# Kernel optimization log

Hardware: AMD Instinct MI355X
Metric: run time of the kernel (lower is better)

## Reference

```python
import jax, jax.numpy as jnp
import numpy as np

B, S, V, NC3, ND = 128, 200, 64, 4000, 100


def setup_inputs() -> dict:
    key = jax.random.key(0)
    ks = jax.random.split(key, 20)
    s = 0.05
    n = lambda k, shp: jax.random.normal(k, shp, dtype=jnp.float32) * s
    return {
        "c3_seq": jax.random.randint(ks[0], (B, S), 0, NC3),
        "d_seq": jax.random.randint(ks[1], (B, S), 0, ND),
        "r_seq": jax.random.randint(ks[2], (B, S), 0, 2),
        "v_c3": n(ks[3], (V,)),
        "D_w": n(ks[4], (ND, 1)),
        "v_d": n(ks[5], (V,)),
        "R_w": n(ks[6], (2, V)),
        "W_ih": n(ks[7], (3 * V, 2 * V)),
        "W_hh": n(ks[8], (3 * V, V)),
        "b_ih": n(ks[9], (3 * V,)),
        "b_hh": n(ks[10], (3 * V,)),
        "l1_w1": n(ks[11], (V, V)),
        "l1_b1": n(ks[12], (V,)),
        "l1_w2": n(ks[13], (1, V)),
        "l1_b2": n(ks[14], (1,)),
        "l2_w1": n(ks[15], (V, 3 * V)),
        "l2_b1": n(ks[16], (V,)),
        "l2_w2": n(ks[17], (1, V)),
        "l2_b2": n(ks[18], (1,)),
    }


def _forward(c3_seq, d_seq, r_seq, v_c3, D_w, v_d, R_w, W_ih, W_hh, b_ih, b_hh,
             l1_w1, l1_b1, l1_w2, l1_b2, l2_w1, l2_b1, l2_w2, l2_b2):
    B_, S_ = c3_seq.shape
    V_ = v_c3.shape[0]
    gamma_seq = D_w[d_seq]                       # [B,S,1]
    v_d_seq = gamma_seq * v_d                    # [B,S,V]
    v_r_seq = R_w[r_seq]                         # [B,S,V]
    x = jnp.concatenate([v_d_seq, v_r_seq], axis=-1)  # [B,S,2V]
    xg = x @ W_ih.T + b_ih                       # precompute GRU input gates [B,S,3V]

    # time-major for scan
    tm = lambda a: jnp.swapaxes(a, 0, 1)
    xg_t, gamma_t = tm(xg), tm(gamma_seq[..., 0])
    r_t, c3_t = tm(r_seq), tm(c3_seq)
    vd_t, vr_t = tm(v_d_seq), tm(v_r_seq)
    rows = jnp.arange(B_)

    def mlp1(h):  # linear_1 (dropout = identity in eval)
        return (jax.nn.relu(h @ l1_w1.T + l1_b1) @ l1_w2.T + l1_b2)[:, 0]

    def mlp2(z):  # linear_2
        return (jax.nn.relu(z @ l2_w1.T + l2_b1) @ l2_w2.T + l2_b2)[:, 0]

    h0 = jnp.zeros((B_, V_), xg.dtype)
    alpha0 = jnp.zeros((B_,), xg.dtype)
    C3_init = jnp.zeros((B_, NC3), xg.dtype)

    def step(carry, inputs):
        h, alpha, C3 = carry
        xg_i, gamma, r, c3, vdi, vri = inputs
        # GRU cell (torch gate order: r, z, n)
        hg = h @ W_hh.T + b_hh
        rg = jax.nn.sigmoid(xg_i[:, :V_] + hg[:, :V_])
        zg = jax.nn.sigmoid(xg_i[:, V_:2 * V_] + hg[:, V_:2 * V_])
        ng = jnp.tanh(xg_i[:, 2 * V_:] + rg * hg[:, 2 * V_:])
        h = (1.0 - zg) * ng + zg * h
        # alpha update
        alpha_new = mlp1(h)
        cond = (alpha - gamma) >= 0
        alpha = jnp.where(r == 1,
                          jnp.where(cond, alpha_new, alpha),
                          jnp.where(cond, alpha, alpha_new))
        # gather -> tiny MLP -> scatter
        beta = C3[rows, c3]                              # [B]
        z = jnp.concatenate([beta[:, None] * v_c3, vdi, vri], axis=-1)  # [B,3V]
        new_c3 = mlp2(z)
        C3 = C3.at[rows, c3].set(new_c3)
        return (h, alpha, C3), (h, alpha, C3)

    _, (h_seq, alpha_seq, C3_seq) = jax.lax.scan(
        step, (h0, alpha0, C3_init), (xg_t, gamma_t, r_t, c3_t, vd_t, vr_t))
    return tm(alpha_seq), tm(h_seq), tm(C3_seq)


def reference(c3_seq, d_seq, r_seq, v_c3, D_w, v_d, R_w, W_ih, W_hh, b_ih, b_hh,
              l1_w1, l1_b1, l1_w2, l1_b2, l2_w1, l2_b1, l2_w2, l2_b2):
    return _forward(c3_seq, d_seq, r_seq, v_c3, D_w, v_d, R_w, W_ih, W_hh, b_ih, b_hh,
                    l1_w1, l1_b1, l1_w2, l1_b2, l2_w1, l2_b1, l2_w2, l2_b2)
```

## Files before the change

### kernel.cpp

```cpp
#include <hip/hip_runtime.h>
#include <math.h>

#define Bn 128
#define Sn 200
#define NC3n 4000
#define GRUB Bn
#define FILLB (Bn * 4)

__device__ __forceinline__ float fexp(float x) { return __builtin_amdgcn_exp2f(x * 1.44269504f); }
__device__ __forceinline__ float frcp(float x) { return __builtin_amdgcn_rcpf(x); }
__device__ __forceinline__ float fsig(float x) { return frcp(1.f + fexp(-x)); }
__device__ __forceinline__ float rlanef(float v, int k) {
    return __int_as_float(__builtin_amdgcn_readlane(__float_as_int(v), k));
}

#define UPD(q, cbase) { int d = cc - (cbase); if ((unsigned)d < 4u) { \
    q.x = (d==0)?v:q.x; q.y = (d==1)?v:q.y; q.z = (d==2)?v:q.z; q.w = (d==3)?v:q.w; } }

struct GruLds {
    float ring[2][16][64];
    float pPart[Sn][4];
    float hbc[4][64];
    float u[192], w0[192], w1[192];
    float hg[2][192];
    float gam[Sn];
    int   r[Sn];
};
struct FillLds {
    float gam[Sn], val[Sn];
    int   r[Sn], c3[Sn], succ[Sn], root[Sn];
    float A[64], Bv[64], C0[64], C1[64], W2[64];
    float l2b2;
};

__global__ __launch_bounds__(256, 2) void fused4_kernel(
    const int* __restrict__ c3_seq, const int* __restrict__ d_seq,
    const int* __restrict__ r_seq, const float* __restrict__ v_c3,
    const float* __restrict__ D_w, const float* __restrict__ v_d,
    const float* __restrict__ R_w, const float* __restrict__ W_ih,
    const float* __restrict__ W_hh, const float* __restrict__ b_ih,
    const float* __restrict__ b_hh,
    const float* __restrict__ l1_w1, const float* __restrict__ l1_b1,
    const float* __restrict__ l1_w2, const float* __restrict__ l1_b2,
    const float* __restrict__ l2_w1, const float* __restrict__ l2_b1,
    const float* __restrict__ l2_w2, const float* __restrict__ l2_b2,
    float* __restrict__ out_alpha, float* __restrict__ out_h,
    float* __restrict__ out_c3)
{
    __shared__ __align__(16) union { GruLds g; FillLds f; } S;

    const int tid = threadIdx.x;
    const int bid = blockIdx.x;

    if (bid < GRUB) {
        __builtin_amdgcn_s_setprio(1);
        const int b    = bid;
        const int role = tid >> 6;
        const int j    = tid & 63;

        if (tid < Sn) {
            S.g.gam[tid] = D_w[d_seq[b * Sn + tid]];
            S.g.r[tid]   = r_seq[b * Sn + tid];
        }
        if (tid < 192) {
            const float4* rp  = (const float4*)(W_ih + (size_t)tid * 128);
            const float4* vd4 = (const float4*)v_d;
            const float4* q04 = (const float4*)R_w;
            const float4* q14 = (const float4*)(R_w + 64);
            float u = 0.f, w0 = 0.f, w1 = 0.f;
            #pragma unroll 4
            for (int k = 0; k < 16; ++k) {
                float4 a  = rp[k];
                float4 bb = rp[16 + k];
                float4 vd = vd4[k], q0 = q04[k], q1 = q14[k];
                u  += a.x*vd.x + a.y*vd.y + a.z*vd.z + a.w*vd.w;
                w0 += bb.x*q0.x + bb.y*q0.y + bb.z*q0.z + bb.w*q0.w;
                w1 += bb.x*q1.x + bb.y*q1.y + bb.z*q1.z + bb.w*q1.w;
            }
            float bih = b_ih[tid];
            S.g.u[tid]  = u;
            S.g.w0[tid] = w0 + bih;
            S.g.w1[tid] = w1 + bih;
        }
        float w[64];
        {
            const float* src = (role < 3) ? (W_hh + (size_t)(role * 64 + j) * 64)
                                          : (l1_w1 + (size_t)j * 64);
            const float4* s4 = (const float4*)src;
            #pragma unroll
            for (int k = 0; k < 16; ++k) {
                float4 v = s4[k];
                w[4*k+0]=v.x; w[4*k+1]=v.y; w[4*k+2]=v.z; w[4*k+3]=v.w;
            }
        }
        float bown = 0.f, l1b = 0.f, l1w2v = 0.f;
        if (role < 3) {
            bown = b_hh[role * 64 + j];
            S.g.hg[0][role * 64 + j] = bown;
        } else {
            l1b = l1_b1[j]; l1w2v = l1_w2[j];
        }
        const float l1b2c = l1_b2[0];
        __syncthreads();

        const float uj  = S.g.u[j],  u1  = S.g.u[64+j],  u2  = S.g.u[128+j];
        const float w00 = S.g.w0[j], w01 = S.g.w0[64+j], w02 = S.g.w0[128+j];
        const float w10 = S.g.w1[j], w11 = S.g.w1[64+j], w12 = S.g.w1[128+j];

        float vh = 0.f;
        float* outh_base = out_h + (size_t)b * Sn * 64;
        const int rloc = 4 * role + (j >> 4);
        const int cloc = (j & 15) * 4;

        for (int t = 0; t < Sn; ++t) {
            if (t && (t & 15) == 0) {
                const int hb = ((t >> 4) & 1) ^ 1;
                float4 v4 = *(const float4*)&S.g.ring[hb][rloc][cloc];
                *(float4*)(outh_base + (size_t)(t - 16 + rloc) * 64 + cloc) = v4;
            }
            const int buf = t & 1;
            float gam = S.g.gam[t];
            int   r   = S.g.r[t];
            float hr = S.g.hg[buf][j], hz = S.g.hg[buf][64+j], hn = S.g.hg[buf][128+j];
            float rg = fsig(fmaf(gam, uj, r ? w10 : w00) + hr);
            float zg = fsig(fmaf(gam, u1, r ? w11 : w01) + hz);
            float e2 = fexp(2.f * (fmaf(gam, u2, r ? w12 : w02) + rg * hn));
            float ng = 1.f - 2.f * frcp(e2 + 1.f);
            vh = (1.f - zg) * ng + zg * vh;
            S.g.hbc[role][j] = vh;
            float4 hreg[16];
            #pragma unroll
            for (int k = 0; k < 16; ++k)
                hreg[k] = *(const float4*)&S.g.hbc[role][k * 4];
            __builtin_amdgcn_sched_barrier(0);
            float a0=0.f, a1=0.f, a2=0.f, a3=0.f;
            #pragma unroll
            for (int k = 0; k < 16; ++k) {
                a0 = fmaf(w[4*k+0], hreg[k].x, a0);
                a1 = fmaf(w[4*k+1], hreg[k].y, a1);
                a2 = fmaf(w[4*k+2], hreg[k].z, a2);
                a3 = fmaf(w[4*k+3], hreg[k].w, a3);
            }
            float dot = (a0 + a1) + (a2 + a3);
            if (role < 3) {
                S.g.hg[buf ^ 1][role * 64 + j] = bown + dot;
            } else {
                float p = fmaxf(dot + l1b, 0.f) * l1w2v;
                p += __shfl_xor(p, 1);
                p += __shfl_xor(p, 2);
                p += __shfl_xor(p, 4);
                p += __shfl_xor(p, 8);
                if ((j & 15) == 0) S.g.pPart[t][j >> 4] = p;
                S.g.ring[(t >> 4) & 1][t & 15][j] = vh;
            }
            __syncthreads();
        }
        if (role < 2) {
            float4 v4 = *(const float4*)&S.g.ring[0][rloc][cloc];
            *(float4*)(outh_base + (size_t)(192 + rloc) * 64 + cloc) = v4;
        }
        if (role == 3) {
            float4 pp0 = *(const float4*)&S.g.pPart[j][0];
            float4 pp1 = *(const float4*)&S.g.pPart[64 + j][0];
            float4 pp2 = *(const float4*)&S.g.pPart[128 + j][0];
            const int j3 = (j < 8) ? (192 + j) : 199;
            float4 pp3 = *(const float4*)&S.g.pPart[j3][0];
            float an0 = ((pp0.x+pp0.y)+(pp0.z+pp0.w)) + l1b2c;
            float an1 = ((pp1.x+pp1.y)+(pp1.z+pp1.w)) + l1b2c;
            float an2 = ((pp2.x+pp2.y)+(pp2.z+pp2.w)) + l1b2c;
            float an3 = ((pp3.x+pp3.y)+(pp3.z+pp3.w)) + l1b2c;
            float g0 = S.g.gam[j],       g1 = S.g.gam[64 + j];
            float g2 = S.g.gam[128 + j], g3 = S.g.gam[j3];
            int   r0 = S.g.r[j],         r1 = S.g.r[64 + j];
            int   r2 = S.g.r[128 + j],   r3 = S.g.r[j3];
            float alpha = 0.f;
            float* oa = out_alpha + b * Sn;
            for (int t = 0; t < Sn; ++t) {
                const int q = t >> 6, l = t & 63;
                float an, g; int rr;
                if (q == 0)      { an = rlanef(an0,l); g = rlanef(g0,l); rr = __builtin_amdgcn_readlane(r0,l); }
                else if (q == 1) { an = rlanef(an1,l); g = rlanef(g1,l); rr = __builtin_amdgcn_readlane(r1,l); }
                else if (q == 2) { an = rlanef(an2,l); g = rlanef(g2,l); rr = __builtin_amdgcn_readlane(r2,l); }
                else             { an = rlanef(an3,l); g = rlanef(g3,l); rr = __builtin_amdgcn_readlane(r3,l); }
                bool cond = (alpha - g) >= 0.f;
                alpha = rr ? (cond ? an : alpha) : (cond ? alpha : an);
                if (j == 0) oa[t] = alpha;
            }
        }
    } else {
        const int fb = bid - GRUB;
        const int b  = fb >> 2;
        const int qt = fb & 3;
        if (tid < Sn) {
            S.f.gam[tid] = D_w[d_seq[b*Sn + tid]];
            S.f.r[tid]   = r_seq[b*Sn + tid];
            S.f.c3[tid]  = c3_seq[b*Sn + tid];
        }
        if (tid < 64) {
            const float4* row4 = (const float4*)(l2_w1 + (size_t)tid * 192);
            const float4* vc4  = (const float4*)v_c3;
            const float4* vd4  = (const float4*)v_d;
            const float4* q04  = (const float4*)R_w;
            const float4* q14  = (const float4*)(R_w + 64);
            float a2=0.f, b2=0.f, c0=0.f, c1=0.f;
            #pragma unroll 4
            for (int k = 0; k < 16; ++k) {
                float4 ra = row4[k], rb = row4[16+k], rc = row4[32+k];
                float4 vc = vc4[k], vd = vd4[k], q0 = q04[k], q1 = q14[k];
                a2 += ra.x*vc.x + ra.y*vc.y + ra.z*vc.z + ra.w*vc.w;
                b2 += rb.x*vd.x + rb.y*vd.y + rb.z*vd.z + rb.w*vd.w;
                c0 += rc.x*q0.x + rc.y*q0.y + rc.z*q0.z + rc.w*q0.w;
                c1 += rc.x*q1.x + rc.y*q1.y + rc.z*q1.z + rc.w*q1.w;
            }
            S.f.A[tid]  = a2;
            S.f.Bv[tid] = b2;
            S.f.C0[tid] = c0 + l2_b1[tid];
            S.f.C1[tid] = c1 + l2_b1[tid];
            S.f.W2[tid] = l2_w2[tid];
        }
        if (tid == 0) S.f.l2b2 = l2_b2[0];
        __syncthreads();
        if (tid < Sn) {
            int c = S.f.c3[tid];
            int s = -1;
            for (int u = tid + 1; u < Sn; ++u)
                if (S.f.c3[u] == c) { s = u; break; }
            S.f.succ[tid] = s;
            int rt = 1;
            for (int u = 0; u < tid; ++u)
                if (S.f.c3[u] == c) { rt = 0; break; }
            S.f.root[tid] = rt;
        }
        __syncthreads();
        {
            const int g  = tid >> 4;
            const int l  = tid & 15;
            const int j0 = l * 4;
            float A0=S.f.A[j0],  A1=S.f.A[j0+1],  A2=S.f.A[j0+2],  A3=S.f.A[j0+3];
            float B0=S.f.Bv[j0], B1=S.f.Bv[j0+1], B2=S.f.Bv[j0+2], B3=S.f.Bv[j0+3];
            float C00=S.f.C0[j0],C01=S.f.C0[j0+1],C02=S.f.C0[j0+2],C03=S.f.C0[j0+3];
            float C10=S.f.C1[j0],C11=S.f.C1[j0+1],C12=S.f.C1[j0+2],C13=S.f.C1[j0+3];
            float W0=S.f.W2[j0], W1=S.f.W2[j0+1], W2v=S.f.W2[j0+2],W3=S.f.W2[j0+3];
            float l2b2 = S.f.l2b2;
            for (int t0 = g; t0 < Sn; t0 += 16) {
                if (!S.f.root[t0]) continue;
                float beta = 0.f;
                int t = t0;
                while (t >= 0) {
                    float gam = S.f.gam[t];
                    int   r   = S.f.r[t];
                    float s = W0*fmaxf(A0*beta + B0*gam + (r ? C10 : C00), 0.f)
                            + W1*fmaxf(A1*beta + B1*gam + (r ? C11 : C01), 0.f)
                            + W2v*fmaxf(A2*beta + B2*gam + (r ? C12 : C02), 0.f)
                            + W3*fmaxf(A3*beta + B3*gam + (r ? C13 : C03), 0.f);
                    s += __shfl_xor(s, 1, 16);
                    s += __shfl_xor(s, 2, 16);
                    s += __shfl_xor(s, 4, 16);
                    s += __shfl_xor(s, 8, 16);
                    beta = s + l2b2;
                    if (l == 0) S.f.val[t] = beta;
                    t = S.f.succ[t];
                }
            }
        }
        __syncthreads();
        const int cA = tid*4, cB = 1024 + tid*4, cC = 2048 + tid*4, cD = 3072 + tid*4;
        float4 qA = make_float4(0.f,0.f,0.f,0.f), qB = qA, qC = qA, qD = qA;
        const int t0 = qt * 50;
        for (int t = 0; t < t0; ++t) {
            int cc = S.f.c3[t]; float v = S.f.val[t];
            UPD(qA, cA) UPD(qB, cB) UPD(qC, cC) UPD(qD, cD)
        }
        float* rowp = out_c3 + (size_t)b * Sn * NC3n + (size_t)t0 * NC3n;
        const bool doD = (tid < 232);
        for (int t = t0; t < t0 + 50; ++t) {
            int cc = S.f.c3[t]; float v = S.f.val[t];
            UPD(qA, cA) UPD(qB, cB) UPD(qC, cC) UPD(qD, cD)
            *(float4*)(rowp + cA) = qA;
            *(float4*)(rowp + cB) = qB;
            *(float4*)(rowp + cC) = qC;
            if (doD) *(float4*)(rowp + cD) = qD;
            rowp += NC3n;
        }
    }
}

extern "C" void kernel_launch(void* const* d_in, const int* in_sizes, int n_in,
                              void* d_out, int out_size, void* d_ws, size_t ws_size,
                              hipStream_t stream)
{
    const int*   c3_seq = (const int*)  d_in[0];
    const int*   d_seq  = (const int*)  d_in[1];
    const int*   r_seq  = (const int*)  d_in[2];
    const float* v_c3   = (const float*)d_in[3];
    const float* D_w    = (const float*)d_in[4];
    const float* v_d    = (const float*)d_in[5];
    const float* R_w    = (const float*)d_in[6];
    const float* W_ih   = (const float*)d_in[7];
    const float* W_hh   = (const float*)d_in[8];
    const float* b_ih   = (const float*)d_in[9];
    const float* b_hh   = (const float*)d_in[10];
    const float* l1_w1  = (const float*)d_in[11];
    const float* l1_b1  = (const float*)d_in[12];
    const float* l1_w2  = (const float*)d_in[13];
    const float* l1_b2  = (const float*)d_in[14];
    const float* l2_w1  = (const float*)d_in[15];
    const float* l2_b1  = (const float*)d_in[16];
    const float* l2_w2  = (const float*)d_in[17];
    const float* l2_b2  = (const float*)d_in[18];

    float* out_alpha = (float*)d_out;
    float* out_h     = out_alpha + Bn*Sn;
    float* out_c3    = out_h + (size_t)Bn*Sn*64;

    fused4_kernel<<<GRUB + FILLB, 256, 0, stream>>>(
        c3_seq, d_seq, r_seq, v_c3, D_w, v_d, R_w, W_ih, W_hh, b_ih, b_hh,
        l1_w1, l1_b1, l1_w2, l1_b2, l2_w1, l2_b1, l2_w2, l2_b2,
        out_alpha, out_h, out_c3);
}
```

Baseline: 161.2 us.

## Run GRU recurrence in a single wavefront and split C3 fill six ways

The GRU block shrinks from four wavefronts to one 64-lane wavefront. Each lane holds all four weight rows (r, z, n and the l1 MLP) in registers, so the per-step __syncthreads and the LDS hand-off of gate pre-activations go away, and h is written straight to global memory each step. The C3 fill blocks become single wavefronts too, with six time-slices per batch row; each lane keeps sixteen float4 running rows and updates them through a switch. The cost is much higher register pressure (over 256 weight floats per lane, which may spill), serial dot products per lane, and redundant chain walking in every fill block.

```diff
diff --git a/kernel.cpp b/kernel.cpp
--- a/kernel.cpp
+++ b/kernel.cpp
@@ -5,7 +5,7 @@
 #define Sn 200
 #define NC3n 4000
 #define GRUB Bn
-#define FILLB (Bn * 4)
+#define FILLB (Bn * 6)
 
 __device__ __forceinline__ float fexp(float x) { return __builtin_amdgcn_exp2f(x * 1.44269504f); }
 __device__ __forceinline__ float frcp(float x) { return __builtin_amdgcn_rcpf(x); }
@@ -14,15 +14,9 @@
     return __int_as_float(__builtin_amdgcn_readlane(__float_as_int(v), k));
 }
 
-#define UPD(q, cbase) { int d = cc - (cbase); if ((unsigned)d < 4u) { \
-    q.x = (d==0)?v:q.x; q.y = (d==1)?v:q.y; q.z = (d==2)?v:q.z; q.w = (d==3)?v:q.w; } }
-
 struct GruLds {
-    float ring[2][16][64];
-    float pPart[Sn][4];
-    float hbc[4][64];
-    float u[192], w0[192], w1[192];
-    float hg[2][192];
+    float hbc[64];
+    float pP[Sn];
     float gam[Sn];
     int   r[Sn];
 };
@@ -33,7 +27,7 @@
     float l2b2;
 };
 
-__global__ __launch_bounds__(256, 2) void fused4_kernel(
+__global__ __launch_bounds__(64, 1) void fused6_kernel(
     const int* __restrict__ c3_seq, const int* __restrict__ d_seq,
     const int* __restrict__ r_seq, const float* __restrict__ v_c3,
     const float* __restrict__ D_w, const float* __restrict__ v_d,
@@ -53,17 +47,15 @@
     const int bid = blockIdx.x;
 
     if (bid < GRUB) {
-        __builtin_amdgcn_s_setprio(1);
-        const int b    = bid;
-        const int role = tid >> 6;
-        const int j    = tid & 63;
-
-        if (tid < Sn) {
-            S.g.gam[tid] = D_w[d_seq[b * Sn + tid]];
-            S.g.r[tid]   = r_seq[b * Sn + tid];
-        }
-        if (tid < 192) {
-            const float4* rp  = (const float4*)(W_ih + (size_t)tid * 128);
+        const int b = bid, j = tid;
+        for (int i = j; i < Sn; i += 64) {
+            S.g.gam[i] = D_w[d_seq[b * Sn + i]];
+            S.g.r[i]   = r_seq[b * Sn + i];
+        }
+        float uu[3], ww0[3], ww1[3];
+        #pragma unroll
+        for (int g = 0; g < 3; ++g) {
+            const float4* rp  = (const float4*)(W_ih + (size_t)(g * 64 + j) * 128);
             const float4* vd4 = (const float4*)v_d;
             const float4* q04 = (const float4*)R_w;
             const float4* q14 = (const float4*)(R_w + 64);
@@ -77,98 +69,79 @@
                 w0 += bb.x*q0.x + bb.y*q0.y + bb.z*q0.z + bb.w*q0.w;
                 w1 += bb.x*q1.x + bb.y*q1.y + bb.z*q1.z + bb.w*q1.w;
             }
-            float bih = b_ih[tid];
-            S.g.u[tid]  = u;
-            S.g.w0[tid] = w0 + bih;
-            S.g.w1[tid] = w1 + bih;
-        }
-        float w[64];
+            float bih = b_ih[g * 64 + j];
+            uu[g] = u; ww0[g] = w0 + bih; ww1[g] = w1 + bih;
+        }
+        float wr[64], wz[64], wn[64], l1r[64];
         {
-            const float* src = (role < 3) ? (W_hh + (size_t)(role * 64 + j) * 64)
-                                          : (l1_w1 + (size_t)j * 64);
-            const float4* s4 = (const float4*)src;
+            const float4* r0 = (const float4*)(W_hh + (size_t)j * 64);
+            const float4* r1 = (const float4*)(W_hh + (size_t)(64 + j) * 64);
+            const float4* r2 = (const float4*)(W_hh + (size_t)(128 + j) * 64);
+            const float4* r3 = (const float4*)(l1_w1 + (size_t)j * 64);
             #pragma unroll
             for (int k = 0; k < 16; ++k) {
-                float4 v = s4[k];
-                w[4*k+0]=v.x; w[4*k+1]=v.y; w[4*k+2]=v.z; w[4*k+3]=v.w;
-            }
-        }
-        float bown = 0.f, l1b = 0.f, l1w2v = 0.f;
-        if (role < 3) {
-            bown = b_hh[role * 64 + j];
-            S.g.hg[0][role * 64 + j] = bown;
-        } else {
-            l1b = l1_b1[j]; l1w2v = l1_w2[j];
-        }
-        const float l1b2c = l1_b2[0];
-        __syncthreads();
-
-        const float uj  = S.g.u[j],  u1  = S.g.u[64+j],  u2  = S.g.u[128+j];
-        const float w00 = S.g.w0[j], w01 = S.g.w0[64+j], w02 = S.g.w0[128+j];
-        const float w10 = S.g.w1[j], w11 = S.g.w1[64+j], w12 = S.g.w1[128+j];
-
+                float4 a = r0[k], c = r1[k], d = r2[k], e = r3[k];
+                wr[4*k+0]=a.x; wr[4*k+1]=a.y; wr[4*k+2]=a.z; wr[4*k+3]=a.w;
+                wz[4*k+0]=c.x; wz[4*k+1]=c.y; wz[4*k+2]=c.z; wz[4*k+3]=c.w;
+                wn[4*k+0]=d.x; wn[4*k+1]=d.y; wn[4*k+2]=d.z; wn[4*k+3]=d.w;
+                l1r[4*k+0]=e.x; l1r[4*k+1]=e.y; l1r[4*k+2]=e.z; l1r[4*k+3]=e.w;
+            }
+        }
+        const float bhr = b_hh[j], bhz = b_hh[64 + j], bhn = b_hh[128 + j];
+        const float l1b = l1_b1[j], l1w2v = l1_w2[j], l1b2c = l1_b2[0];
+
+        float hgr = bhr, hgz = bhz, hgn = bhn;
         float vh = 0.f;
-        float* outh_base = out_h + (size_t)b * Sn * 64;
-        const int rloc = 4 * role + (j >> 4);
-        const int cloc = (j & 15) * 4;
+        float* outp = out_h + (size_t)b * Sn * 64 + j;
+        float gamc = S.g.gam[0]; int rc = S.g.r[0];
 
         for (int t = 0; t < Sn; ++t) {
-            if (t && (t & 15) == 0) {
-                const int hb = ((t >> 4) & 1) ^ 1;
-                float4 v4 = *(const float4*)&S.g.ring[hb][rloc][cloc];
-                *(float4*)(outh_base + (size_t)(t - 16 + rloc) * 64 + cloc) = v4;
-            }
-            const int buf = t & 1;
-            float gam = S.g.gam[t];
-            int   r   = S.g.r[t];
-            float hr = S.g.hg[buf][j], hz = S.g.hg[buf][64+j], hn = S.g.hg[buf][128+j];
-            float rg = fsig(fmaf(gam, uj, r ? w10 : w00) + hr);
-            float zg = fsig(fmaf(gam, u1, r ? w11 : w01) + hz);
-            float e2 = fexp(2.f * (fmaf(gam, u2, r ? w12 : w02) + rg * hn));
+            float gam = gamc; int r = rc;
+            float rg = fsig(fmaf(gam, uu[0], r ? ww1[0] : ww0[0]) + hgr);
+            float zg = fsig(fmaf(gam, uu[1], r ? ww1[1] : ww0[1]) + hgz);
+            float e2 = fexp(2.f * (fmaf(gam, uu[2], r ? ww1[2] : ww0[2]) + rg * hgn));
             float ng = 1.f - 2.f * frcp(e2 + 1.f);
             vh = (1.f - zg) * ng + zg * vh;
-            S.g.hbc[role][j] = vh;
+            outp[0] = vh; outp += 64;
+            S.g.hbc[j] = vh;
             float4 hreg[16];
             #pragma unroll
             for (int k = 0; k < 16; ++k)
-                hreg[k] = *(const float4*)&S.g.hbc[role][k * 4];
+                hreg[k] = *(const float4*)&S.g.hbc[k * 4];
             __builtin_amdgcn_sched_barrier(0);
-            float a0=0.f, a1=0.f, a2=0.f, a3=0.f;
+            if (t + 1 < Sn) { gamc = S.g.gam[t + 1]; rc = S.g.r[t + 1]; }
+            float ar0=0,ar1=0,ar2=0,ar3=0, az0=0,az1=0,az2=0,az3=0;
+            float an0=0,an1=0,an2=0,an3=0, am0=0,am1=0,am2=0,am3=0;
             #pragma unroll
             for (int k = 0; k < 16; ++k) {
-                a0 = fmaf(w[4*k+0], hreg[k].x, a0);
-                a1 = fmaf(w[4*k+1], hreg[k].y, a1);
-                a2 = fmaf(w[4*k+2], hreg[k].z, a2);
-                a3 = fmaf(w[4*k+3], hreg[k].w, a3);
-            }
-            float dot = (a0 + a1) + (a2 + a3);
-            if (role < 3) {
-                S.g.hg[buf ^ 1][role * 64 + j] = bown + dot;
-            } else {
-                float p = fmaxf(dot + l1b, 0.f) * l1w2v;
-                p += __shfl_xor(p, 1);
-                p += __shfl_xor(p, 2);
-                p += __shfl_xor(p, 4);
-                p += __shfl_xor(p, 8);
-                if ((j & 15) == 0) S.g.pPart[t][j >> 4] = p;
-                S.g.ring[(t >> 4) & 1][t & 15][j] = vh;
-            }
-            __syncthreads();
-        }
-        if (role < 2) {
-            float4 v4 = *(const float4*)&S.g.ring[0][rloc][cloc];
-            *(float4*)(outh_base + (size_t)(192 + rloc) * 64 + cloc) = v4;
-        }
-        if (role == 3) {
-            float4 pp0 = *(const float4*)&S.g.pPart[j][0];
-            float4 pp1 = *(const float4*)&S.g.pPart[64 + j][0];
-            float4 pp2 = *(const float4*)&S.g.pPart[128 + j][0];
+                float4 h4 = hreg[k];
+                ar0 = fmaf(wr[4*k+0], h4.x, ar0); ar1 = fmaf(wr[4*k+1], h4.y, ar1);
+                ar2 = fmaf(wr[4*k+2], h4.z, ar2); ar3 = fmaf(wr[4*k+3], h4.w, ar3);
+                az0 = fmaf(wz[4*k+0], h4.x, az0); az1 = fmaf(wz[4*k+1], h4.y, az1);
+                az2 = fmaf(wz[4*k+2], h4.z, az2); az3 = fmaf(wz[4*k+3], h4.w, az3);
+                an0 = fmaf(wn[4*k+0], h4.x, an0); an1 = fmaf(wn[4*k+1], h4.y, an1);
+                an2 = fmaf(wn[4*k+2], h4.z, an2); an3 = fmaf(wn[4*k+3], h4.w, an3);
+                am0 = fmaf(l1r[4*k+0], h4.x, am0); am1 = fmaf(l1r[4*k+1], h4.y, am1);
+                am2 = fmaf(l1r[4*k+2], h4.z, am2); am3 = fmaf(l1r[4*k+3], h4.w, am3);
+            }
+            hgr = bhr + ((ar0+ar1)+(ar2+ar3));
+            hgz = bhz + ((az0+az1)+(az2+az3));
+            hgn = bhn + ((an0+an1)+(an2+an3));
+            float p = fmaxf(((am0+am1)+(am2+am3)) + l1b, 0.f) * l1w2v;
+            p += __shfl_xor(p, 1);
+            p += __shfl_xor(p, 2);
+            p += __shfl_xor(p, 4);
+            p += __shfl_xor(p, 8);
+            p += __shfl_xor(p, 16);
+            p += __shfl_xor(p, 32);
+            if (j == 0) S.g.pP[t] = p;
+        }
+        {
             const int j3 = (j < 8) ? (192 + j) : 199;
-            float4 pp3 = *(const float4*)&S.g.pPart[j3][0];
-            float an0 = ((pp0.x+pp0.y)+(pp0.z+pp0.w)) + l1b2c;
-            float an1 = ((pp1.x+pp1.y)+(pp1.z+pp1.w)) + l1b2c;
-            float an2 = ((pp2.x+pp2.y)+(pp2.z+pp2.w)) + l1b2c;
-            float an3 = ((pp3.x+pp3.y)+(pp3.z+pp3.w)) + l1b2c;
+            float an0 = S.g.pP[j]       + l1b2c;
+            float an1 = S.g.pP[64 + j]  + l1b2c;
+            float an2 = S.g.pP[128 + j] + l1b2c;
+            float an3 = S.g.pP[j3]      + l1b2c;
             float g0 = S.g.gam[j],       g1 = S.g.gam[64 + j];
             float g2 = S.g.gam[128 + j], g3 = S.g.gam[j3];
             int   r0 = S.g.r[j],         r1 = S.g.r[64 + j];
@@ -189,14 +162,16 @@
         }
     } else {
         const int fb = bid - GRUB;
-        const int b  = fb >> 2;
-        const int qt = fb & 3;
-        if (tid < Sn) {
-            S.f.gam[tid] = D_w[d_seq[b*Sn + tid]];
-            S.f.r[tid]   = r_seq[b*Sn + tid];
-            S.f.c3[tid]  = c3_seq[b*Sn + tid];
-        }
-        if (tid < 64) {
+        const int b  = fb / 6;
+        const int sp = fb - b * 6;
+        const int t0 = sp * 33 + (sp < 2 ? sp : 2);
+        const int t1 = t0 + (sp < 2 ? 34 : 33);
+        for (int i = tid; i < Sn; i += 64) {
+            S.f.gam[i] = D_w[d_seq[b*Sn + i]];
+            S.f.r[i]   = r_seq[b*Sn + i];
+            S.f.c3[i]  = c3_seq[b*Sn + i];
+        }
+        {
             const float4* row4 = (const float4*)(l2_w1 + (size_t)tid * 192);
             const float4* vc4  = (const float4*)v_c3;
             const float4* vd4  = (const float4*)v_d;
@@ -217,21 +192,19 @@
             S.f.C0[tid] = c0 + l2_b1[tid];
             S.f.C1[tid] = c1 + l2_b1[tid];
             S.f.W2[tid] = l2_w2[tid];
-        }
-        if (tid == 0) S.f.l2b2 = l2_b2[0];
-        __syncthreads();
-        if (tid < Sn) {
-            int c = S.f.c3[tid];
+            if (tid == 0) S.f.l2b2 = l2_b2[0];
+        }
+        for (int i = tid; i < Sn; i += 64) {
+            int c = S.f.c3[i];
             int s = -1;
-            for (int u = tid + 1; u < Sn; ++u)
+            for (int u = i + 1; u < Sn; ++u)
                 if (S.f.c3[u] == c) { s = u; break; }
-            S.f.succ[tid] = s;
+            S.f.succ[i] = s;
             int rt = 1;
-            for (int u = 0; u < tid; ++u)
+            for (int u = 0; u < i; ++u)
                 if (S.f.c3[u] == c) { rt = 0; break; }
-            S.f.root[tid] = rt;
-        }
-        __syncthreads();
+            S.f.root[i] = rt;
+        }
         {
             const int g  = tid >> 4;
             const int l  = tid & 15;
@@ -242,10 +215,10 @@
             float C10=S.f.C1[j0],C11=S.f.C1[j0+1],C12=S.f.C1[j0+2],C13=S.f.C1[j0+3];
             float W0=S.f.W2[j0], W1=S.f.W2[j0+1], W2v=S.f.W2[j0+2],W3=S.f.W2[j0+3];
             float l2b2 = S.f.l2b2;
-            for (int t0 = g; t0 < Sn; t0 += 16) {
-                if (!S.f.root[t0]) continue;
+            for (int tt = g; tt < Sn; tt += 4) {
+                if (!S.f.root[tt]) continue;
                 float beta = 0.f;
-                int t = t0;
+                int t = tt;
                 while (t >= 0) {
                     float gam = S.f.gam[t];
                     int   r   = S.f.r[t];
@@ -263,23 +236,56 @@
                 }
             }
         }
-        __syncthreads();
-        const int cA = tid*4, cB = 1024 + tid*4, cC = 2048 + tid*4, cD = 3072 + tid*4;
-        float4 qA = make_float4(0.f,0.f,0.f,0.f), qB = qA, qC = qA, qD = qA;
-        const int t0 = qt * 50;
+        float4 st0,st1,st2,st3,st4,st5,st6,st7,st8,st9,st10,st11,st12,st13,st14,st15;
+        st0=st1=st2=st3=st4=st5=st6=st7=st8=st9=st10=st11=st12=st13=st14=st15
+            = make_float4(0.f,0.f,0.f,0.f);
+        const unsigned base = (unsigned)(tid * 4);
+        #define FUPD() { unsigned rel = (unsigned)cc - base;                                 \
+            if (rel < 4096u && (rel & 255u) < 4u) {                                          \
+                const int q = rel >> 8, d = rel & 3; const float v = vv;                     \
+                switch (q) {                                                                 \
+                case 0:  st0.x=(d==0)?v:st0.x;  st0.y=(d==1)?v:st0.y;  st0.z=(d==2)?v:st0.z;  st0.w=(d==3)?v:st0.w;  break; \
+                case 1:  st1.x=(d==0)?v:st1.x;  st1.y=(d==1)?v:st1.y;  st1.z=(d==2)?v:st1.z;  st1.w=(d==3)?v:st1.w;  break; \
+                case 2:  st2.x=(d==0)?v:st2.x;  st2.y=(d==1)?v:st2.y;  st2.z=(d==2)?v:st2.z;  st2.w=(d==3)?v:st2.w;  break; \
+                case 3:  st3.x=(d==0)?v:st3.x;  st3.y=(d==1)?v:st3.y;  st3.z=(d==2)?v:st3.z;  st3.w=(d==3)?v:st3.w;  break; \
+                case 4:  st4.x=(d==0)?v:st4.x;  st4.y=(d==1)?v:st4.y;  st4.z=(d==2)?v:st4.z;  st4.w=(d==3)?v:st4.w;  break; \
+                case 5:  st5.x=(d==0)?v:st5.x;  st5.y=(d==1)?v:st5.y;  st5.z=(d==2)?v:st5.z;  st5.w=(d==3)?v:st5.w;  break; \
+                case 6:  st6.x=(d==0)?v:st6.x;  st6.y=(d==1)?v:st6.y;  st6.z=(d==2)?v:st6.z;  st6.w=(d==3)?v:st6.w;  break; \
+                case 7:  st7.x=(d==0)?v:st7.x;  st7.y=(d==1)?v:st7.y;  st7.z=(d==2)?v:st7.z;  st7.w=(d==3)?v:st7.w;  break; \
+                case 8:  st8.x=(d==0)?v:st8.x;  st8.y=(d==1)?v:st8.y;  st8.z=(d==2)?v:st8.z;  st8.w=(d==3)?v:st8.w;  break; \
+                case 9:  st9.x=(d==0)?v:st9.x;  st9.y=(d==1)?v:st9.y;  st9.z=(d==2)?v:st9.z;  st9.w=(d==3)?v:st9.w;  break; \
+                case 10: st10.x=(d==0)?v:st10.x; st10.y=(d==1)?v:st10.y; st10.z=(d==2)?v:st10.z; st10.w=(d==3)?v:st10.w; break; \
+                case 11: st11.x=(d==0)?v:st11.x; st11.y=(d==1)?v:st11.y; st11.z=(d==2)?v:st11.z; st11.w=(d==3)?v:st11.w; break; \
+                case 12: st12.x=(d==0)?v:st12.x; st12.y=(d==1)?v:st12.y; st12.z=(d==2)?v:st12.z; st12.w=(d==3)?v:st12.w; break; \
+                case 13: st13.x=(d==0)?v:st13.x; st13.y=(d==1)?v:st13.y; st13.z=(d==2)?v:st13.z; st13.w=(d==3)?v:st13.w; break; \
+                case 14: st14.x=(d==0)?v:st14.x; st14.y=(d==1)?v:st14.y; st14.z=(d==2)?v:st14.z; st14.w=(d==3)?v:st14.w; break; \
+                default: st15.x=(d==0)?v:st15.x; st15.y=(d==1)?v:st15.y; st15.z=(d==2)?v:st15.z; st15.w=(d==3)?v:st15.w; break; \
+                } } }
         for (int t = 0; t < t0; ++t) {
-            int cc = S.f.c3[t]; float v = S.f.val[t];
-            UPD(qA, cA) UPD(qB, cB) UPD(qC, cC) UPD(qD, cD)
+            int cc = S.f.c3[t]; float vv = S.f.val[t];
+            FUPD()
         }
         float* rowp = out_c3 + (size_t)b * Sn * NC3n + (size_t)t0 * NC3n;
-        const bool doD = (tid < 232);
-        for (int t = t0; t < t0 + 50; ++t) {
-            int cc = S.f.c3[t]; float v = S.f.val[t];
-            UPD(qA, cA) UPD(qB, cB) UPD(qC, cC) UPD(qD, cD)
-            *(float4*)(rowp + cA) = qA;
-            *(float4*)(rowp + cB) = qB;
-            *(float4*)(rowp + cC) = qC;
-            if (doD) *(float4*)(rowp + cD) = qD;
+        for (int t = t0; t < t1; ++t) {
+            int cc = S.f.c3[t]; float vv = S.f.val[t];
+            FUPD()
+            float* lp = rowp + tid * 4;
+            *(float4*)(lp + 0*256)  = st0;
+            *(float4*)(lp + 1*256)  = st1;
+            *(float4*)(lp + 2*256)  = st2;
+            *(float4*)(lp + 3*256)  = st3;
+            *(float4*)(lp + 4*256)  = st4;
+            *(float4*)(lp + 5*256)  = st5;
+            *(float4*)(lp + 6*256)  = st6;
+            *(float4*)(lp + 7*256)  = st7;
+            *(float4*)(lp + 8*256)  = st8;
+            *(float4*)(lp + 9*256)  = st9;
+            *(float4*)(lp + 10*256) = st10;
+            *(float4*)(lp + 11*256) = st11;
+            *(float4*)(lp + 12*256) = st12;
+            *(float4*)(lp + 13*256) = st13;
+            *(float4*)(lp + 14*256) = st14;
+            if (tid < 40) *(float4*)(lp + 15*256) = st15;
             rowp += NC3n;
         }
     }
@@ -313,7 +319,7 @@
     float* out_h     = out_alpha + Bn*Sn;
     float* out_c3    = out_h + (size_t)Bn*Sn*64;
 
-    fused4_kernel<<<GRUB + FILLB, 256, 0, stream>>>(
+    fused6_kernel<<<GRUB + FILLB, 64, 0, stream>>>(
         c3_seq, d_seq, r_seq, v_c3, D_w, v_d, R_w, W_ih, W_hh, b_ih, b_hh,
         l1_w1, l1_b1, l1_w2, l1_b2, l2_w1, l2_b1, l2_w2, l2_b2,
         out_alpha, out_h, out_c3);
```

Result: slower. 250.8 us (+55.5%).

## Use 512-thread blocks: two GRU rows per block, two fill blocks per batch

Applied to the files above, without the earlier changes.

Blocks grow to 512 threads. Each GRU block now runs two batch rows, each with its own shared-memory state, and the two recurrences share one block-wide barrier per step. The fill of the large per-step C3 state tensor is split into two halves of 100 timesteps per batch instead of four quarters of 50, so less prefix replay is repeated across blocks. The cost is that two independent recurrences are locked together on every barrier, the GRU priority hint is dropped, and occupancy changes with the 512-thread, one-block launch bound.

```diff
diff --git a/kernel.cpp b/kernel.cpp
--- a/kernel.cpp
+++ b/kernel.cpp
@@ -4,8 +4,8 @@
 #define Bn 128
 #define Sn 200
 #define NC3n 4000
-#define GRUB Bn
-#define FILLB (Bn * 4)
+#define GRUB 64
+#define FILLB (Bn * 2)
 
 __device__ __forceinline__ float fexp(float x) { return __builtin_amdgcn_exp2f(x * 1.44269504f); }
 __device__ __forceinline__ float frcp(float x) { return __builtin_amdgcn_rcpf(x); }
@@ -33,7 +33,7 @@
     float l2b2;
 };
 
-__global__ __launch_bounds__(256, 2) void fused4_kernel(
+__global__ __launch_bounds__(512, 1) void fused7_kernel(
     const int* __restrict__ c3_seq, const int* __restrict__ d_seq,
     const int* __restrict__ r_seq, const float* __restrict__ v_c3,
     const float* __restrict__ D_w, const float* __restrict__ v_d,
@@ -47,23 +47,25 @@
     float* __restrict__ out_alpha, float* __restrict__ out_h,
     float* __restrict__ out_c3)
 {
-    __shared__ __align__(16) union { GruLds g; FillLds f; } S;
+    __shared__ __align__(16) union { GruLds g[2]; FillLds f; } S;
 
     const int tid = threadIdx.x;
     const int bid = blockIdx.x;
 
     if (bid < GRUB) {
-        __builtin_amdgcn_s_setprio(1);
-        const int b    = bid;
-        const int role = tid >> 6;
+        const int rw   = tid >> 8;
+        const int role = (tid >> 6) & 3;
         const int j    = tid & 63;
-
-        if (tid < Sn) {
-            S.g.gam[tid] = D_w[d_seq[b * Sn + tid]];
-            S.g.r[tid]   = r_seq[b * Sn + tid];
-        }
-        if (tid < 192) {
-            const float4* rp  = (const float4*)(W_ih + (size_t)tid * 128);
+        const int ht   = tid & 255;
+        const int b    = bid * 2 + rw;
+        GruLds& G = S.g[rw];
+
+        if (ht < Sn) {
+            G.gam[ht] = D_w[d_seq[b * Sn + ht]];
+            G.r[ht]   = r_seq[b * Sn + ht];
+        }
+        if (ht < 192) {
+            const float4* rp  = (const float4*)(W_ih + (size_t)ht * 128);
             const float4* vd4 = (const float4*)v_d;
             const float4* q04 = (const float4*)R_w;
             const float4* q14 = (const float4*)(R_w + 64);
@@ -77,10 +79,10 @@
                 w0 += bb.x*q0.x + bb.y*q0.y + bb.z*q0.z + bb.w*q0.w;
                 w1 += bb.x*q1.x + bb.y*q1.y + bb.z*q1.z + bb.w*q1.w;
             }
-            float bih = b_ih[tid];
-            S.g.u[tid]  = u;
-            S.g.w0[tid] = w0 + bih;
-            S.g.w1[tid] = w1 + bih;
+            float bih = b_ih[ht];
+            G.u[ht]  = u;
+            G.w0[ht] = w0 + bih;
+            G.w1[ht] = w1 + bih;
         }
         float w[64];
         {
@@ -96,16 +98,16 @@
         float bown = 0.f, l1b = 0.f, l1w2v = 0.f;
         if (role < 3) {
             bown = b_hh[role * 64 + j];
-            S.g.hg[0][role * 64 + j] = bown;
+            G.hg[0][role * 64 + j] = bown;
         } else {
             l1b = l1_b1[j]; l1w2v = l1_w2[j];
         }
         const float l1b2c = l1_b2[0];
         __syncthreads();
 
-        const float uj  = S.g.u[j],  u1  = S.g.u[64+j],  u2  = S.g.u[128+j];
-        const float w00 = S.g.w0[j], w01 = S.g.w0[64+j], w02 = S.g.w0[128+j];
-        const float w10 = S.g.w1[j], w11 = S.g.w1[64+j], w12 = S.g.w1[128+j];
+        const float uj  = G.u[j],  u1  = G.u[64+j],  u2  = G.u[128+j];
+        const float w00 = G.w0[j], w01 = G.w0[64+j], w02 = G.w0[128+j];
+        const float w10 = G.w1[j], w11 = G.w1[64+j], w12 = G.w1[128+j];
 
         float vh = 0.f;
         float* outh_base = out_h + (size_t)b * Sn * 64;
@@ -115,23 +117,23 @@
         for (int t = 0; t < Sn; ++t) {
             if (t && (t & 15) == 0) {
                 const int hb = ((t >> 4) & 1) ^ 1;
-                float4 v4 = *(const float4*)&S.g.ring[hb][rloc][cloc];
+                float4 v4 = *(const float4*)&G.ring[hb][rloc][cloc];
                 *(float4*)(outh_base + (size_t)(t - 16 + rloc) * 64 + cloc) = v4;
             }
             const int buf = t & 1;
-            float gam = S.g.gam[t];
-            int   r   = S.g.r[t];
-            float hr = S.g.hg[buf][j], hz = S.g.hg[buf][64+j], hn = S.g.hg[buf][128+j];
+            float gam = G.gam[t];
+            int   r   = G.r[t];
+            float hr = G.hg[buf][j], hz = G.hg[buf][64+j], hn = G.hg[buf][128+j];
             float rg = fsig(fmaf(gam, uj, r ? w10 : w00) + hr);
             float zg = fsig(fmaf(gam, u1, r ? w11 : w01) + hz);
             float e2 = fexp(2.f * (fmaf(gam, u2, r ? w12 : w02) + rg * hn));
             float ng = 1.f - 2.f * frcp(e2 + 1.f);
             vh = (1.f - zg) * ng + zg * vh;
-            S.g.hbc[role][j] = vh;
+            G.hbc[role][j] = vh;
             float4 hreg[16];
             #pragma unroll
             for (int k = 0; k < 16; ++k)
-                hreg[k] = *(const float4*)&S.g.hbc[role][k * 4];
+                hreg[k] = *(const float4*)&G.hbc[role][k * 4];
             __builtin_amdgcn_sched_barrier(0);
             float a0=0.f, a1=0.f, a2=0.f, a3=0.f;
             #pragma unroll
@@ -143,36 +145,36 @@
             }
             float dot = (a0 + a1) + (a2 + a3);
             if (role < 3) {
-                S.g.hg[buf ^ 1][role * 64 + j] = bown + dot;
+                G.hg[buf ^ 1][role * 64 + j] = bown + dot;
             } else {
                 float p = fmaxf(dot + l1b, 0.f) * l1w2v;
                 p += __shfl_xor(p, 1);
                 p += __shfl_xor(p, 2);
                 p += __shfl_xor(p, 4);
                 p += __shfl_xor(p, 8);
-                if ((j & 15) == 0) S.g.pPart[t][j >> 4] = p;
-                S.g.ring[(t >> 4) & 1][t & 15][j] = vh;
+                if ((j & 15) == 0) G.pPart[t][j >> 4] = p;
+                G.ring[(t >> 4) & 1][t & 15][j] = vh;
             }
             __syncthreads();
         }
         if (role < 2) {
-            float4 v4 = *(const float4*)&S.g.ring[0][rloc][cloc];
+            float4 v4 = *(const float4*)&G.ring[0][rloc][cloc];
             *(float4*)(outh_base + (size_t)(192 + rloc) * 64 + cloc) = v4;
         }
         if (role == 3) {
-            float4 pp0 = *(const float4*)&S.g.pPart[j][0];
-            float4 pp1 = *(const float4*)&S.g.pPart[64 + j][0];
-            float4 pp2 = *(const float4*)&S.g.pPart[128 + j][0];
+            float4 pp0 = *(const float4*)&G.pPart[j][0];
+            float4 pp1 = *(const float4*)&G.pPart[64 + j][0];
+            float4 pp2 = *(const float4*)&G.pPart[128 + j][0];
             const int j3 = (j < 8) ? (192 + j) : 199;
-            float4 pp3 = *(const float4*)&S.g.pPart[j3][0];
+            float4 pp3 = *(const float4*)&G.pPart[j3][0];
             float an0 = ((pp0.x+pp0.y)+(pp0.z+pp0.w)) + l1b2c;
             float an1 = ((pp1.x+pp1.y)+(pp1.z+pp1.w)) + l1b2c;
             float an2 = ((pp2.x+pp2.y)+(pp2.z+pp2.w)) + l1b2c;
             float an3 = ((pp3.x+pp3.y)+(pp3.z+pp3.w)) + l1b2c;
-            float g0 = S.g.gam[j],       g1 = S.g.gam[64 + j];
-            float g2 = S.g.gam[128 + j], g3 = S.g.gam[j3];
-            int   r0 = S.g.r[j],         r1 = S.g.r[64 + j];
-            int   r2 = S.g.r[128 + j],   r3 = S.g.r[j3];
+            float g0 = G.gam[j],       g1 = G.gam[64 + j];
+            float g2 = G.gam[128 + j], g3 = G.gam[j3];
+            int   r0 = G.r[j],         r1 = G.r[64 + j];
+            int   r2 = G.r[128 + j],   r3 = G.r[j3];
             float alpha = 0.f;
             float* oa = out_alpha + b * Sn;
             for (int t = 0; t < Sn; ++t) {
@@ -188,9 +190,9 @@
             }
         }
     } else {
-        const int fb = bid - GRUB;
-        const int b  = fb >> 2;
-        const int qt = fb & 3;
+        const int fb   = bid - GRUB;
+        const int b    = fb >> 1;
+        const int half = fb & 1;
         if (tid < Sn) {
             S.f.gam[tid] = D_w[d_seq[b*Sn + tid]];
             S.f.r[tid]   = r_seq[b*Sn + tid];
@@ -232,7 +234,7 @@
             S.f.root[tid] = rt;
         }
         __syncthreads();
-        {
+        if (tid < 256) {
             const int g  = tid >> 4;
             const int l  = tid & 15;
             const int j0 = l * 4;
@@ -264,23 +266,22 @@
             }
         }
         __syncthreads();
-        const int cA = tid*4, cB = 1024 + tid*4, cC = 2048 + tid*4, cD = 3072 + tid*4;
-        float4 qA = make_float4(0.f,0.f,0.f,0.f), qB = qA, qC = qA, qD = qA;
-        const int t0 = qt * 50;
-        for (int t = 0; t < t0; ++t) {
-            int cc = S.f.c3[t]; float v = S.f.val[t];
-            UPD(qA, cA) UPD(qB, cB) UPD(qC, cC) UPD(qD, cD)
-        }
-        float* rowp = out_c3 + (size_t)b * Sn * NC3n + (size_t)t0 * NC3n;
-        const bool doD = (tid < 232);
-        for (int t = t0; t < t0 + 50; ++t) {
-            int cc = S.f.c3[t]; float v = S.f.val[t];
-            UPD(qA, cA) UPD(qB, cB) UPD(qC, cC) UPD(qD, cD)
-            *(float4*)(rowp + cA) = qA;
-            *(float4*)(rowp + cB) = qB;
-            *(float4*)(rowp + cC) = qC;
-            if (doD) *(float4*)(rowp + cD) = qD;
-            rowp += NC3n;
+        if (tid < 500) {
+            const int cA = tid * 4, cB = 2000 + tid * 4;
+            float4 qA = make_float4(0.f,0.f,0.f,0.f), qB = qA;
+            const int t0 = half * 100;
+            for (int t = 0; t < t0; ++t) {
+                int cc = S.f.c3[t]; float v = S.f.val[t];
+                UPD(qA, cA) UPD(qB, cB)
+            }
+            float* rowp = out_c3 + (size_t)b * Sn * NC3n + (size_t)t0 * NC3n;
+            for (int t = t0; t < t0 + 100; ++t) {
+                int cc = S.f.c3[t]; float v = S.f.val[t];
+                UPD(qA, cA) UPD(qB, cB)
+                *(float4*)(rowp + cA) = qA;
+                *(float4*)(rowp + cB) = qB;
+                rowp += NC3n;
+            }
         }
     }
 }
@@ -313,7 +314,7 @@
     float* out_h     = out_alpha + Bn*Sn;
     float* out_c3    = out_h + (size_t)Bn*Sn*64;
 
-    fused4_kernel<<<GRUB + FILLB, 256, 0, stream>>>(
+    fused7_kernel<<<GRUB + FILLB, 512, 0, stream>>>(
         c3_seq, d_seq, r_seq, v_c3, D_w, v_d, R_w, W_ih, W_hh, b_ih, b_hh,
         l1_w1, l1_b1, l1_w2, l1_b2, l2_w1, l2_b1, l2_w2, l2_b2,
         out_alpha, out_h, out_c3);
```

After: 183.8 us. 14.0% more time.
